# Kernel optimization log

Hardware: AMD Instinct MI355X
Metric: run time of the kernel (lower is better)

## Reference

```python
import jax, jax.numpy as jnp
import numpy as np
import math

N, IFZ, NVZ, AHZ, QPZ, KZ, PEZ = 1024, 256, 64, 8, 4, 20, 20
NUM_FREQ = PEZ // 2
FREQ_INV = 50.0

def layer_norm(x, g, b, eps=1e-5):
    mu = x.mean(-1, keepdims=True)
    var = ((x - mu) ** 2).mean(-1, keepdims=True)
    return (x - mu) / jnp.sqrt(var + eps) * g + b

def setup_inputs() -> dict:
    key = jax.random.key(0)
    ks = jax.random.split(key, 8)
    x = jax.random.normal(ks[0], (N, IFZ), jnp.float32)
    affines = jax.random.normal(ks[1], (N, 3, 4), jnp.float32)
    prot_mask = jnp.ones((N,), dtype=bool)
    edge_index = jax.random.randint(ks[2], (N, KZ), 0, N, dtype=jnp.int32)
    s = 0.02
    w_nde = jax.random.normal(ks[3], (KZ * 3 * PEZ, NVZ), jnp.float32) * s
    b_nde = jnp.zeros((NVZ,), jnp.float32)
    w_q = jax.random.normal(ks[4], (IFZ + NVZ, AHZ * QPZ * 3), jnp.float32) * s
    w_v = jax.random.normal(ks[5], (IFZ + NVZ, AHZ * QPZ * IFZ), jnp.float32) * s
    ln_ag_g = jnp.ones((AHZ * QPZ * IFZ,), jnp.float32)
    ln_ag_b = jnp.zeros((AHZ * QPZ * IFZ,), jnp.float32)
    w_ag = jax.random.normal(ks[6], (AHZ * QPZ * IFZ, IFZ), jnp.float32) * s
    ln_en_g = jnp.ones((IFZ,), jnp.float32)
    ln_en_b = jnp.zeros((IFZ,), jnp.float32)
    return dict(x=x, affines=affines, prot_mask=prot_mask, edge_index=edge_index,
                w_nde=w_nde, b_nde=b_nde, w_q=w_q, w_v=w_v,
                ln_ag_g=ln_ag_g, ln_ag_b=ln_ag_b, w_ag=w_ag,
                ln_en_g=ln_en_g, ln_en_b=ln_en_b)

def reference(x, affines, prot_mask, edge_index, w_nde, b_nde, w_q, w_v,
              ln_ag_g, ln_ag_b, w_ag, ln_en_g, ln_en_b):
    dtype = x.dtype
    R = affines[:, :, :3]                                   # (N,3,3) rotation
    t = affines[:, :, 3]                                    # (N,3) translation
    positions = t
    # --- BackboneDistanceEmbedding (reconstructed): local neighbour vectors ---
    rel = positions[edge_index] - t[:, None, :]             # (N,K,3)
    local = jnp.einsum('nji,nkj->nki', R, rel)              # inverse-affine (R^T) (N,K,3)
    freqs = jnp.arange(1, NUM_FREQ + 1, dtype=dtype) / FREQ_INV
    ang = local[..., None] * freqs                          # (N,K,3,F)
    pe = jnp.concatenate([jnp.sin(ang), jnp.cos(ang)], -1)  # (N,K,3,PEZ)
    nv = jax.nn.relu(pe.reshape(x.shape[0], -1) @ w_nde + b_nde)  # (N,NVZ)
    nv = nv * prot_mask[:, None].astype(dtype)
    x_ne = jnp.concatenate([x, nv], axis=-1)                # (N,IFZ+NVZ)
    # --- query points in global frame ---
    q = (x_ne @ w_q).reshape(-1, 1, AHZ, QPZ, 3)
    q = jnp.einsum('nij,nkaqj->nkaqi', R, q) + t[:, None, None, None, :]
    gnp = positions[edge_index][:, :, None, None, :]        # (N,K,1,1,3)
    # --- L2-distance attention over neighbourhood ---
    scores = -jnp.linalg.norm(q - gnp, axis=-1).sum(-1)     # (N,K,AHZ)
    attn = jax.nn.softmax(scores, axis=1).astype(dtype)
    # --- value gather + weighted aggregation ---
    v = (x_ne @ w_v).reshape(-1, AHZ, QPZ, IFZ)
    v_ne = v[edge_index]                                    # (N,K,AHZ,QPZ,IFZ) -- big gather
    new = jnp.einsum('nkaqi,nka->naqi', v_ne, attn).reshape(x.shape[0], -1)
    new = layer_norm(new, ln_ag_g, ln_ag_b) @ w_ag          # dropout: eval mode => identity
    out = layer_norm(x + new / math.sqrt(2.0), ln_en_g, ln_en_b).astype(dtype)
    return out, edge_index
```

## Files before the change

### kernel.cpp

```cpp
#include <hip/hip_runtime.h>
#include <hip/hip_bf16.h>
#include <math.h>

#define NNODE 1024
#define IFZ   256
#define NVZ   64
#define AHZ   8
#define QPZ   4
#define KZ    20
#define PEZ   20
#define NF    10
#define XNE   320
#define VROW  8192
#define PEK   1280
#define SPLITS 8

typedef unsigned short ushort;
typedef __attribute__((ext_vector_type(8))) short    short8v;
typedef __attribute__((ext_vector_type(8))) ushort   ushort8v;
typedef __attribute__((ext_vector_type(4))) float    float4v;

static __device__ __forceinline__ ushort f2bf(float f) {
    unsigned u = __float_as_uint(f);
    unsigned r = 0x7FFFu + ((u >> 16) & 1u);
    return (ushort)((u + r) >> 16);
}
static __device__ __forceinline__ float bf2f(unsigned h) {
    return __uint_as_float(h << 16);
}

struct TJob { const float* src; ushort* dst; const float* scl;
              int R, C, gx, base, Rdst; };
struct TJobs { TJob j[4]; };

__global__ __launch_bounds__(256) void t_conv_all(TJobs P)
{
    const int bid = blockIdx.x;
    int ji = 0;
    #pragma unroll
    for (int t = 1; t < 4; ++t) if (bid >= P.j[t].base) ji = t;
    const TJob jb = P.j[ji];
    const int rel = bid - jb.base;
    const int bx = rel % jb.gx, by = rel / jb.gx;

    __shared__ float t[32][33];
    const int c0 = bx * 32, r0 = by * 32;
    const int tx = threadIdx.x, ty = threadIdx.y;
    #pragma unroll
    for (int i = 0; i < 4; ++i) {
        int r = r0 + ty + 8*i, c = c0 + tx;
        float v = (r < jb.R && c < jb.C) ? jb.src[(size_t)r * jb.C + c] : 0.f;
        if (jb.scl && r < jb.R) v *= jb.scl[r];
        t[ty + 8*i][tx] = v;
    }
    __syncthreads();
    #pragma unroll
    for (int i = 0; i < 4; ++i)
        jb.dst[(size_t)(c0 + ty + 8*i) * jb.Rdst + r0 + tx] = f2bf(t[tx][ty + 8*i]);
}

__global__ __launch_bounds__(256) void k_gemv(
    const float* __restrict__ wag, const float* __restrict__ g,
    const float* __restrict__ b, float* __restrict__ vpart)
{
    const int sp = blockIdx.x, j = threadIdx.x;
    const float* base = wag + (size_t)sp * 128 * IFZ;
    float vp = 0.f, bp = 0.f;
    for (int r = 0; r < 128; ++r) {
        float w = base[(size_t)r * IFZ + j];
        vp += g[sp*128 + r] * w;
        bp += b[sp*128 + r] * w;
    }
    vpart[(size_t)(sp*2 + 0) * IFZ + j] = vp;
    vpart[(size_t)(sp*2 + 1) * IFZ + j] = bp;
}

__global__ __launch_bounds__(64) void k0_geom(
    const float* __restrict__ x, const float* __restrict__ aff,
    const int* __restrict__ edge,
    ushort* __restrict__ pe, ushort* __restrict__ xne_out,
    float* __restrict__ geom)
{
    const int n = blockIdx.x;
    const int lane = threadIdx.x;
    __shared__ float tn[KZ][3];
    __shared__ float r9[9], tt[3];

    if (lane < KZ) {
        int e = edge[n*KZ + lane];
        float a0 = aff[e*12 + 3], a1 = aff[e*12 + 7], a2 = aff[e*12 + 11];
        tn[lane][0] = a0; tn[lane][1] = a1; tn[lane][2] = a2;
        geom[n*72 + 12 + lane*3 + 0] = a0;
        geom[n*72 + 12 + lane*3 + 1] = a1;
        geom[n*72 + 12 + lane*3 + 2] = a2;
    } else if (lane < 29) {
        int q = lane - 20;
        float v = aff[n*12 + (q/3)*4 + (q%3)];
        r9[q] = v;
        geom[n*72 + q] = v;
    } else if (lane < 32) {
        float v = aff[n*12 + (lane-29)*4 + 3];
        tt[lane-29] = v;
        geom[n*72 + 9 + (lane-29)] = v;
    }
    {
        float4 xv = ((const float4*)(x + (size_t)n*IFZ))[lane];
        unsigned lo = f2bf(xv.x) | ((unsigned)f2bf(xv.y) << 16);
        unsigned hi = f2bf(xv.z) | ((unsigned)f2bf(xv.w) << 16);
        unsigned* p = (unsigned*)(xne_out + (size_t)n*XNE) + lane*2;
        p[0] = lo; p[1] = hi;
    }
    __syncthreads();

    if (lane < 60) {
        int k = lane / 3, i = lane % 3;
        float r0 = tn[k][0]-tt[0], r1 = tn[k][1]-tt[1], r2 = tn[k][2]-tt[2];
        float loc = r9[0+i]*r0 + r9[3+i]*r1 + r9[6+i]*r2;
        size_t base = (size_t)n*PEK + k*60 + i*20;
        #pragma unroll
        for (int p = 0; p < NF; p += 2) {
            float a0 = loc * (float)(p+1) * (1.0f/50.0f);
            float a1 = loc * (float)(p+2) * (1.0f/50.0f);
            unsigned us = f2bf(__sinf(a0)) | ((unsigned)f2bf(__sinf(a1)) << 16);
            unsigned uc = f2bf(__cosf(a0)) | ((unsigned)f2bf(__cosf(a1)) << 16);
            *(unsigned*)&pe[base + p]      = us;
            *(unsigned*)&pe[base + 10 + p] = uc;
        }
    }
    if (lane < 40)
        *(unsigned*)&pe[(size_t)n*PEK + 1200 + lane*2] = 0u;
}

#define EPI_F32S 1

template<int EPI>
__global__ __launch_bounds__(256) void gemm_bt(
    const ushort* __restrict__ A, const ushort* __restrict__ BT,
    ushort* __restrict__ Cb, float* __restrict__ Cf,
    const float* __restrict__ bias, int K, int ksplit, int ldc)
{
    __shared__ ushort As[64][40];
    __shared__ ushort Bs[64][40];
    const int bm = blockIdx.y * 64;
    const int bn = blockIdx.x * 64;
    const int tid = threadIdx.x;
    const int w = tid >> 6, lane = tid & 63;
    const int wr = w >> 1, wc = w & 1;
    const int lane15 = lane & 15, quad = lane >> 4;
    const int kbeg = blockIdx.z * ksplit;
    const int kend = kbeg + ksplit;

    const int sm = tid >> 2;
    const int sk = (tid & 3) * 8;

    float4v acc[2][2] = {};
    for (int k0 = kbeg; k0 < kend; k0 += 32) {
        *(ushort8v*)&As[sm][sk] = *(const ushort8v*)&A[(size_t)(bm + sm)*K + k0 + sk];
        *(ushort8v*)&Bs[sm][sk] = *(const ushort8v*)&BT[(size_t)(bn + sm)*K + k0 + sk];
        __syncthreads();
        short8v a0 = *(const short8v*)&As[wr*32      + lane15][quad*8];
        short8v a1 = *(const short8v*)&As[wr*32 + 16 + lane15][quad*8];
        short8v b0 = *(const short8v*)&Bs[wc*32      + lane15][quad*8];
        short8v b1 = *(const short8v*)&Bs[wc*32 + 16 + lane15][quad*8];
        acc[0][0] = __builtin_amdgcn_mfma_f32_16x16x32_bf16(a0, b0, acc[0][0], 0, 0, 0);
        acc[0][1] = __builtin_amdgcn_mfma_f32_16x16x32_bf16(a0, b1, acc[0][1], 0, 0, 0);
        acc[1][0] = __builtin_amdgcn_mfma_f32_16x16x32_bf16(a1, b0, acc[1][0], 0, 0, 0);
        acc[1][1] = __builtin_amdgcn_mfma_f32_16x16x32_bf16(a1, b1, acc[1][1], 0, 0, 0);
        __syncthreads();
    }

    const size_t splitoff = (size_t)blockIdx.z * (size_t)NNODE * (size_t)ldc;
    #pragma unroll
    for (int i = 0; i < 2; ++i) {
        #pragma unroll
        for (int j = 0; j < 2; ++j) {
            int col = bn + wc*32 + j*16 + lane15;
            #pragma unroll
            for (int r = 0; r < 4; ++r) {
                int row = bm + wr*32 + i*16 + quad*4 + r;
                Cf[splitoff + (size_t)row*ldc + col] = acc[i][j][r];
            }
        }
    }
}

__global__ __launch_bounds__(256) void gemm_head(
    const ushort* __restrict__ Ab, const ushort* __restrict__ BTb,
    ushort* __restrict__ C, float2* __restrict__ spart)
{
    const int a = blockIdx.z;
    const ushort* A  = Ab  + (size_t)a * 1024 * XNE;
    const ushort* BT = BTb + (size_t)a * 1024 * XNE;
    __shared__ ushort As[64][40];
    __shared__ ushort Bs[64][40];
    const int bm = blockIdx.y * 64;
    const int bn = blockIdx.x * 64;
    const int tid = threadIdx.x;
    const int w = tid >> 6, lane = tid & 63;
    const int wr = w >> 1, wc = w & 1;
    const int lane15 = lane & 15, quad = lane >> 4;
    const int sm = tid >> 2;
    const int sk = (tid & 3) * 8;

    float4v acc[2][2] = {};
    for (int k0 = 0; k0 < XNE; k0 += 32) {
        *(ushort8v*)&As[sm][sk] = *(const ushort8v*)&A[(size_t)(bm + sm)*XNE + k0 + sk];
        *(ushort8v*)&Bs[sm][sk] = *(const ushort8v*)&BT[(size_t)(bn + sm)*XNE + k0 + sk];
        __syncthreads();
        short8v a0 = *(const short8v*)&As[wr*32      + lane15][quad*8];
        short8v a1 = *(const short8v*)&As[wr*32 + 16 + lane15][quad*8];
        short8v b0 = *(const short8v*)&Bs[wc*32      + lane15][quad*8];
        short8v b1 = *(const short8v*)&Bs[wc*32 + 16 + lane15][quad*8];
        acc[0][0] = __builtin_amdgcn_mfma_f32_16x16x32_bf16(a0, b0, acc[0][0], 0, 0, 0);
        acc[0][1] = __builtin_amdgcn_mfma_f32_16x16x32_bf16(a0, b1, acc[0][1], 0, 0, 0);
        acc[1][0] = __builtin_amdgcn_mfma_f32_16x16x32_bf16(a1, b0, acc[1][0], 0, 0, 0);
        acc[1][1] = __builtin_amdgcn_mfma_f32_16x16x32_bf16(a1, b1, acc[1][1], 0, 0, 0);
        __syncthreads();
    }

    float rs[2][4], rq[2][4];
    #pragma unroll
    for (int i = 0; i < 2; ++i)
        #pragma unroll
        for (int r = 0; r < 4; ++r) {
            float v0 = acc[i][0][r], v1 = acc[i][1][r];
            rs[i][r] = v0 + v1;
            rq[i][r] = v0*v0 + v1*v1;
        }
    #pragma unroll
    for (int m = 1; m < 16; m <<= 1) {
        #pragma unroll
        for (int i = 0; i < 2; ++i)
            #pragma unroll
            for (int r = 0; r < 4; ++r) {
                rs[i][r] += __shfl_xor(rs[i][r], m, 64);
                rq[i][r] += __shfl_xor(rq[i][r], m, 64);
            }
    }
    if (lane15 == 0) {
        const int slot = a*32 + bn/32  ;
        const int slot2 = a*32 + (bn >> 5) + wc;
        (void)slot;
        #pragma unroll
        for (int i = 0; i < 2; ++i)
            #pragma unroll
            for (int r = 0; r < 4; ++r) {
                int row = bm + wr*32 + i*16 + quad*4 + r;
                spart[(size_t)row*256 + slot2] = make_float2(rs[i][r], rq[i][r]);
            }
    }

    #pragma unroll
    for (int i = 0; i < 2; ++i) {
        #pragma unroll
        for (int j = 0; j < 2; ++j) {
            int col = a*1024 + bn + wc*32 + j*16 + lane15;
            #pragma unroll
            for (int r = 0; r < 4; ++r) {
                int row = bm + wr*32 + i*16 + quad*4 + r;
                C[(size_t)row*VROW + col] = f2bf(acc[i][j][r]);
            }
        }
    }
}

__global__ __launch_bounds__(256) void k_nv(
    const float* __restrict__ nvpart, const float* __restrict__ bias,
    const float* __restrict__ vpart, ushort* __restrict__ xne,
    float* __restrict__ vconst)
{
    const int tid = threadIdx.x;
    if (blockIdx.x >= 256) {
        int vb = blockIdx.x - 256;
        float s = 0.f;
        #pragma unroll 8
        for (int sp = 0; sp < 64; ++sp)
            s += vpart[(size_t)(sp*2 + vb)*IFZ + tid];
        vconst[vb*IFZ + tid] = s;
        return;
    }
    int idx = blockIdx.x*256 + tid;
    int n = idx >> 6, c = idx & 63;
    float s = nvpart[idx] + nvpart[65536 + idx] + nvpart[2*65536 + idx]
            + nvpart[3*65536 + idx];
    xne[(size_t)n*XNE + IFZ + c] = f2bf(fmaxf(s + bias[c], 0.f));
}

__global__ __launch_bounds__(256) void k_sc_agg(
    const float* __restrict__ qbuf, const float* __restrict__ geom,
    const ushort* __restrict__ xne, const int* __restrict__ edge,
    ushort* __restrict__ agg)
{
    const int n = blockIdx.x;
    const int tid = threadIdx.x;
    __shared__ float geo[72], qg[96], sc[160], at[160];
    __shared__ int es[KZ];
    __shared__ ushort xs[KZ][XNE];

    if (tid < 72) geo[tid] = geom[n*72 + tid];
    else if (tid < 92) es[tid-72] = edge[n*KZ + (tid-72)];
    __syncthreads();

    if (tid < 96) {
        int i = tid % 3, base = (tid/3)*3;
        float q0 = qbuf[n*128 + base], q1 = qbuf[n*128 + base+1], q2 = qbuf[n*128 + base+2];
        qg[tid] = geo[i*3+0]*q0 + geo[i*3+1]*q1 + geo[i*3+2]*q2 + geo[9+i];
    }
    for (int s = tid; s < KZ*40; s += 256) {
        int k = s / 40, ch = s % 40;
        *(ushort8v*)&xs[k][ch*8] = *(const ushort8v*)&xne[(size_t)es[k]*XNE + ch*8];
    }
    __syncthreads();

    if (tid < 160) {
        int k = tid / 8, a = tid % 8;
        float tx = geo[12+k*3+0], ty = geo[12+k*3+1], tz = geo[12+k*3+2];
        float acc = 0.f;
        #pragma unroll
        for (int qp = 0; qp < QPZ; ++qp) {
            int b = a*12 + qp*3;
            float dx = qg[b]   - tx;
            float dy = qg[b+1] - ty;
            float dz = qg[b+2] - tz;
            acc += sqrtf(dx*dx + dy*dy + dz*dz);
        }
        sc[a*20 + k] = -acc;
    }
    __syncthreads();
    if (tid < 8) {
        int a = tid;
        float m = -1e30f;
        #pragma unroll
        for (int k = 0; k < KZ; ++k) m = fmaxf(m, sc[a*20+k]);
        float e[KZ]; float sum = 0.f;
        #pragma unroll
        for (int k = 0; k < KZ; ++k) { e[k] = __expf(sc[a*20+k] - m); sum += e[k]; }
        float inv = 1.f / sum;
        #pragma unroll
        for (int k = 0; k < KZ; ++k) at[k*8 + a] = e[k]*inv;
    }
    __syncthreads();

    for (int s = tid; s < AHZ*40; s += 256) {
        int a = s / 40, ch = s % 40;
        float acc[8] = {};
        #pragma unroll 4
        for (int k = 0; k < KZ; ++k) {
            ushort8v p = *(const ushort8v*)&xs[k][ch*8];
            float wgt = at[k*8 + a];
            #pragma unroll
            for (int j = 0; j < 8; ++j)
                acc[j] += wgt * bf2f((ushort)p[j]);
        }
        ushort8v o;
        #pragma unroll
        for (int j = 0; j < 8; ++j) o[j] = (short)f2bf(acc[j]);
        *(ushort8v*)&agg[((size_t)a*NNODE + n)*XNE + ch*8] = o;
    }
}

__global__ __launch_bounds__(256) void k6_final(
    const float* __restrict__ x, const float* __restrict__ tmp,
    const float* __restrict__ g, const float* __restrict__ b,
    const int* __restrict__ edge, const float2* __restrict__ spart,
    const float* __restrict__ vconst, float* __restrict__ out)
{
    const int n = blockIdx.x;
    const int tid = threadIdx.x;
    __shared__ float wsum[4], wsq[4];
    __shared__ float s_mu8, s_rstd8, s_mu, s_rstd;
    const int wid = tid >> 6, lane = tid & 63;

    float2 sp = spart[(size_t)n*256 + tid];
    float a8 = sp.x, q8 = sp.y;
    #pragma unroll
    for (int off = 32; off > 0; off >>= 1) {
        a8 += __shfl_down(a8, off, 64);
        q8 += __shfl_down(q8, off, 64);
    }
    if (lane == 0) { wsum[wid] = a8; wsq[wid] = q8; }
    __syncthreads();
    if (tid == 0) {
        float ts = wsum[0]+wsum[1]+wsum[2]+wsum[3];
        float tq = wsq[0]+wsq[1]+wsq[2]+wsq[3];
        float mu = ts * (1.f/(float)VROW);
        float var = tq * (1.f/(float)VROW) - mu*mu;
        s_mu8 = mu; s_rstd8 = rsqrtf(var + 1e-5f);
    }
    __syncthreads();
    const float mu8 = s_mu8, rstd8 = s_rstd8;

    float s = 0.f;
    #pragma unroll
    for (int spi = 0; spi < SPLITS; ++spi)
        s += tmp[spi*(NNODE*IFZ) + n*IFZ + tid];
    float vc = vconst[tid], bc = vconst[IFZ + tid];
    float pre = rstd8*s - rstd8*mu8*vc + bc;

    float val = x[n*IFZ + tid] + pre * 0.70710678118654752f;
    float lsum = val, lsq = val*val;
    #pragma unroll
    for (int off = 32; off > 0; off >>= 1) {
        lsum += __shfl_down(lsum, off, 64);
        lsq  += __shfl_down(lsq,  off, 64);
    }
    __syncthreads();
    if (lane == 0) { wsum[wid] = lsum; wsq[wid] = lsq; }
    __syncthreads();
    if (tid == 0) {
        float ts = wsum[0]+wsum[1]+wsum[2]+wsum[3];
        float tq = wsq[0]+wsq[1]+wsq[2]+wsq[3];
        float mu = ts / (float)IFZ;
        float var = tq / (float)IFZ - mu*mu;
        s_mu = mu; s_rstd = rsqrtf(var + 1e-5f);
    }
    __syncthreads();
    out[n*IFZ + tid] = (val - s_mu)*s_rstd*g[tid] + b[tid];
    if (tid < KZ)
        out[NNODE*IFZ + n*KZ + tid] = (float)edge[n*KZ + tid];
}

extern "C" void kernel_launch(void* const* d_in, const int* in_sizes, int n_in,
                              void* d_out, int out_size, void* d_ws, size_t ws_size,
                              hipStream_t stream)
{
    const float* x       = (const float*)d_in[0];
    const float* aff     = (const float*)d_in[1];
    const int*   edge    = (const int*)d_in[3];
    const float* w_nde   = (const float*)d_in[4];
    const float* b_nde   = (const float*)d_in[5];
    const float* w_q     = (const float*)d_in[6];
    const float* w_v     = (const float*)d_in[7];
    const float* ln_ag_g = (const float*)d_in[8];
    const float* ln_ag_b = (const float*)d_in[9];
    const float* w_ag    = (const float*)d_in[10];
    const float* ln_en_g = (const float*)d_in[11];
    const float* ln_en_b = (const float*)d_in[12];
    float* out = (float*)d_out;
    char*  w   = (char*)d_ws;

    ushort* xne_bf = (ushort*)(w + 0x0);
    float2* spart  = (float2*)(w + 0xA0000);
    float*  vpart  = (float*) (w + 0x2A0000);
    float*  vconst = (float*) (w + 0x2C0000);
    float*  nvpart = (float*) (w + 0x2D0000);
    ushort* wvT    = (ushort*)(w + 0x3D0000);
    ushort* wagT   = (ushort*)(w + 0x8D0000);
    ushort* newbf  = (ushort*)(w + 0xCD0000);
    float*  tmpk   = (float*) (w + 0x1CD0000);
    ushort* pebf   = (ushort*)(w + 0x24D0000);
    ushort* wndeT  = (ushort*)(w + 0x2750000);
    ushort* wqT    = (ushort*)(w + 0x2778000);
    float*  qbuf   = (float*) (w + 0x278C000);
    float*  geom   = (float*) (w + 0x280C000);
    ushort* agg    = (ushort*)(w + 0x2854000);

    TJobs P;
    P.j[0] = { w_v,   wvT,   nullptr, XNE,  VROW, VROW/32, 0,    XNE  };
    P.j[1] = { w_ag,  wagT,  ln_ag_g, VROW, IFZ,  IFZ/32,  2560, VROW };
    P.j[2] = { w_nde, wndeT, nullptr, 1200, NVZ,  2,       4608, PEK  };
    P.j[3] = { w_q,   wqT,   nullptr, XNE,  96,   4,       4688, XNE  };
    hipLaunchKernelGGL(t_conv_all, dim3(4728), dim3(32, 8), 0, stream, P);

    hipLaunchKernelGGL(k_gemv, dim3(64), dim3(256), 0, stream,
                       w_ag, ln_ag_g, ln_ag_b, vpart);

    hipLaunchKernelGGL(k0_geom, dim3(NNODE), dim3(64), 0, stream,
                       x, aff, edge, pebf, xne_bf, geom);

    hipLaunchKernelGGL((gemm_bt<EPI_F32S>), dim3(1, NNODE/64, 4), dim3(256), 0, stream,
                       pebf, wndeT, (ushort*)nullptr, nvpart, (float*)nullptr,
                       PEK, PEK/4, NVZ);

    hipLaunchKernelGGL(k_nv, dim3(258), dim3(256), 0, stream,
                       nvpart, b_nde, vpart, xne_bf, vconst);

    hipLaunchKernelGGL((gemm_bt<EPI_F32S>), dim3(2, NNODE/64, 1), dim3(256), 0, stream,
                       xne_bf, wqT, (ushort*)nullptr, qbuf, (float*)nullptr,
                       XNE, XNE, 128);

    hipLaunchKernelGGL(k_sc_agg, dim3(NNODE), dim3(256), 0, stream,
                       qbuf, geom, xne_bf, edge, agg);

    hipLaunchKernelGGL(gemm_head, dim3(1024/64, NNODE/64, AHZ), dim3(256), 0, stream,
                       agg, wvT, newbf, spart);

    hipLaunchKernelGGL((gemm_bt<EPI_F32S>), dim3(IFZ/64, NNODE/64, SPLITS), dim3(256), 0, stream,
                       newbf, wagT, (ushort*)nullptr, tmpk, (float*)nullptr,
                       VROW, VROW/SPLITS, IFZ);

    hipLaunchKernelGGL(k6_final, dim3(NNODE), dim3(256), 0, stream,
                       x, tmpk, ln_en_g, ln_en_b, edge, spart, vconst, out);
}
```

Before: 177.0 us.

## Fold value projection into output weights and Gram matrix, merge prep launches

Reassociates the big value path so the 1024x8192 per-head value tensor is never formed. A combined weight WcT = w_v·(g*w_ag) and a per-head Gram matrix G = w_v·w_vᵀ are precomputed. LayerNorm statistics come from row sums of w_v and quadratic forms agg·G·agg, and the output projection is computed directly from the 2560-wide aggregated features. Preprocessing kernels and the small GEMMs are merged into single multi-job launches to cut launch count. The trade-off is extra per-call weight-product GEMMs and possible precision changes in the variance computed via the Gram form.

```diff
diff --git a/kernel.cpp b/kernel.cpp
--- a/kernel.cpp
+++ b/kernel.cpp
@@ -8,12 +8,12 @@
 #define AHZ   8
 #define QPZ   4
 #define KZ    20
-#define PEZ   20
 #define NF    10
 #define XNE   320
 #define VROW  8192
 #define PEK   1280
-#define SPLITS 8
+#define PTOT  2560
+#define SPLITS2 2
 
 typedef unsigned short ushort;
 typedef __attribute__((ext_vector_type(8))) short    short8v;
@@ -29,134 +29,18 @@
     return __uint_as_float(h << 16);
 }
 
-struct TJob { const float* src; ushort* dst; const float* scl;
-              int R, C, gx, base, Rdst; };
-struct TJobs { TJob j[4]; };
-
-__global__ __launch_bounds__(256) void t_conv_all(TJobs P)
-{
-    const int bid = blockIdx.x;
-    int ji = 0;
-    #pragma unroll
-    for (int t = 1; t < 4; ++t) if (bid >= P.j[t].base) ji = t;
-    const TJob jb = P.j[ji];
-    const int rel = bid - jb.base;
-    const int bx = rel % jb.gx, by = rel / jb.gx;
-
-    __shared__ float t[32][33];
-    const int c0 = bx * 32, r0 = by * 32;
-    const int tx = threadIdx.x, ty = threadIdx.y;
-    #pragma unroll
-    for (int i = 0; i < 4; ++i) {
-        int r = r0 + ty + 8*i, c = c0 + tx;
-        float v = (r < jb.R && c < jb.C) ? jb.src[(size_t)r * jb.C + c] : 0.f;
-        if (jb.scl && r < jb.R) v *= jb.scl[r];
-        t[ty + 8*i][tx] = v;
-    }
-    __syncthreads();
-    #pragma unroll
-    for (int i = 0; i < 4; ++i)
-        jb.dst[(size_t)(c0 + ty + 8*i) * jb.Rdst + r0 + tx] = f2bf(t[tx][ty + 8*i]);
-}
-
-__global__ __launch_bounds__(256) void k_gemv(
-    const float* __restrict__ wag, const float* __restrict__ g,
-    const float* __restrict__ b, float* __restrict__ vpart)
-{
-    const int sp = blockIdx.x, j = threadIdx.x;
-    const float* base = wag + (size_t)sp * 128 * IFZ;
-    float vp = 0.f, bp = 0.f;
-    for (int r = 0; r < 128; ++r) {
-        float w = base[(size_t)r * IFZ + j];
-        vp += g[sp*128 + r] * w;
-        bp += b[sp*128 + r] * w;
-    }
-    vpart[(size_t)(sp*2 + 0) * IFZ + j] = vp;
-    vpart[(size_t)(sp*2 + 1) * IFZ + j] = bp;
-}
-
-__global__ __launch_bounds__(64) void k0_geom(
-    const float* __restrict__ x, const float* __restrict__ aff,
-    const int* __restrict__ edge,
-    ushort* __restrict__ pe, ushort* __restrict__ xne_out,
-    float* __restrict__ geom)
-{
-    const int n = blockIdx.x;
-    const int lane = threadIdx.x;
-    __shared__ float tn[KZ][3];
-    __shared__ float r9[9], tt[3];
-
-    if (lane < KZ) {
-        int e = edge[n*KZ + lane];
-        float a0 = aff[e*12 + 3], a1 = aff[e*12 + 7], a2 = aff[e*12 + 11];
-        tn[lane][0] = a0; tn[lane][1] = a1; tn[lane][2] = a2;
-        geom[n*72 + 12 + lane*3 + 0] = a0;
-        geom[n*72 + 12 + lane*3 + 1] = a1;
-        geom[n*72 + 12 + lane*3 + 2] = a2;
-    } else if (lane < 29) {
-        int q = lane - 20;
-        float v = aff[n*12 + (q/3)*4 + (q%3)];
-        r9[q] = v;
-        geom[n*72 + q] = v;
-    } else if (lane < 32) {
-        float v = aff[n*12 + (lane-29)*4 + 3];
-        tt[lane-29] = v;
-        geom[n*72 + 9 + (lane-29)] = v;
-    }
-    {
-        float4 xv = ((const float4*)(x + (size_t)n*IFZ))[lane];
-        unsigned lo = f2bf(xv.x) | ((unsigned)f2bf(xv.y) << 16);
-        unsigned hi = f2bf(xv.z) | ((unsigned)f2bf(xv.w) << 16);
-        unsigned* p = (unsigned*)(xne_out + (size_t)n*XNE) + lane*2;
-        p[0] = lo; p[1] = hi;
-    }
-    __syncthreads();
-
-    if (lane < 60) {
-        int k = lane / 3, i = lane % 3;
-        float r0 = tn[k][0]-tt[0], r1 = tn[k][1]-tt[1], r2 = tn[k][2]-tt[2];
-        float loc = r9[0+i]*r0 + r9[3+i]*r1 + r9[6+i]*r2;
-        size_t base = (size_t)n*PEK + k*60 + i*20;
-        #pragma unroll
-        for (int p = 0; p < NF; p += 2) {
-            float a0 = loc * (float)(p+1) * (1.0f/50.0f);
-            float a1 = loc * (float)(p+2) * (1.0f/50.0f);
-            unsigned us = f2bf(__sinf(a0)) | ((unsigned)f2bf(__sinf(a1)) << 16);
-            unsigned uc = f2bf(__cosf(a0)) | ((unsigned)f2bf(__cosf(a1)) << 16);
-            *(unsigned*)&pe[base + p]      = us;
-            *(unsigned*)&pe[base + 10 + p] = uc;
-        }
-    }
-    if (lane < 40)
-        *(unsigned*)&pe[(size_t)n*PEK + 1200 + lane*2] = 0u;
-}
-
-#define EPI_F32S 1
-
-template<int EPI>
-__global__ __launch_bounds__(256) void gemm_bt(
+static __device__ __forceinline__ void gemm_tile(
     const ushort* __restrict__ A, const ushort* __restrict__ BT,
-    ushort* __restrict__ Cb, float* __restrict__ Cf,
-    const float* __restrict__ bias, int K, int ksplit, int ldc)
-{
-    __shared__ ushort As[64][40];
-    __shared__ ushort Bs[64][40];
-    const int bm = blockIdx.y * 64;
-    const int bn = blockIdx.x * 64;
-    const int tid = threadIdx.x;
+    int aStride, int btStride, int kLen, int bm, int bn, int tid,
+    float4v acc[2][2], ushort (&As)[64][40], ushort (&Bs)[64][40])
+{
     const int w = tid >> 6, lane = tid & 63;
     const int wr = w >> 1, wc = w & 1;
     const int lane15 = lane & 15, quad = lane >> 4;
-    const int kbeg = blockIdx.z * ksplit;
-    const int kend = kbeg + ksplit;
-
-    const int sm = tid >> 2;
-    const int sk = (tid & 3) * 8;
-
-    float4v acc[2][2] = {};
-    for (int k0 = kbeg; k0 < kend; k0 += 32) {
-        *(ushort8v*)&As[sm][sk] = *(const ushort8v*)&A[(size_t)(bm + sm)*K + k0 + sk];
-        *(ushort8v*)&Bs[sm][sk] = *(const ushort8v*)&BT[(size_t)(bn + sm)*K + k0 + sk];
+    const int sm = tid >> 2, sk = (tid & 3) * 8;
+    for (int k0 = 0; k0 < kLen; k0 += 32) {
+        *(ushort8v*)&As[sm][sk] = *(const ushort8v*)&A[(size_t)(bm + sm)*aStride + k0 + sk];
+        *(ushort8v*)&Bs[sm][sk] = *(const ushort8v*)&BT[(size_t)(bn + sm)*btStride + k0 + sk];
         __syncthreads();
         short8v a0 = *(const short8v*)&As[wr*32      + lane15][quad*8];
         short8v a1 = *(const short8v*)&As[wr*32 + 16 + lane15][quad*8];
@@ -168,8 +52,167 @@
         acc[1][1] = __builtin_amdgcn_mfma_f32_16x16x32_bf16(a1, b1, acc[1][1], 0, 0, 0);
         __syncthreads();
     }
-
-    const size_t splitoff = (size_t)blockIdx.z * (size_t)NNODE * (size_t)ldc;
+}
+
+#define T1_END 2048
+#define T2_END 2128
+#define T3_END 2168
+#define CV_END 2488
+#define GV_END 2552
+#define K0_END 2808
+
+__global__ __launch_bounds__(256) void prep(
+    const float* __restrict__ w_ag, const float* __restrict__ ln_ag_g,
+    const float* __restrict__ ln_ag_b,
+    const float* __restrict__ w_nde, const float* __restrict__ w_q,
+    const float* __restrict__ w_v,
+    const float* __restrict__ x, const float* __restrict__ aff,
+    const int* __restrict__ edge,
+    ushort* __restrict__ wagT, ushort* __restrict__ wndeT,
+    ushort* __restrict__ wqT, ushort* __restrict__ wv_bf,
+    float* __restrict__ rsum, float* __restrict__ vpart,
+    ushort* __restrict__ pebf, ushort* __restrict__ xne_bf,
+    float* __restrict__ geom)
+{
+    const int bid = blockIdx.x;
+    const int tid = threadIdx.x;
+
+    __shared__ float t[32][33];
+    __shared__ float part[256];
+    __shared__ float tn[4][KZ][3];
+    __shared__ float r9[4][9], tt[4][3];
+
+    if (bid < T3_END) {
+        const float* src; ushort* dst; const float* scl;
+        int R, C, gx, Rdst, rel;
+        if (bid < T1_END)      { src=w_ag; dst=wagT; scl=ln_ag_g; R=VROW; C=IFZ; gx=8;  Rdst=VROW; rel=bid; }
+        else if (bid < T2_END) { src=w_nde;dst=wndeT;scl=nullptr; R=1200; C=NVZ; gx=2;  Rdst=PEK;  rel=bid-T1_END; }
+        else                   { src=w_q;  dst=wqT;  scl=nullptr; R=XNE;  C=96;  gx=4;  Rdst=XNE;  rel=bid-T2_END; }
+        const int bx = rel % gx, by = rel / gx;
+        const int c0 = bx*32, r0 = by*32;
+        const int tx = tid & 31, ty = tid >> 5;
+        #pragma unroll
+        for (int i = 0; i < 4; ++i) {
+            int r = r0 + ty + 8*i, c = c0 + tx;
+            float v = (r < R && c < C) ? src[(size_t)r * C + c] : 0.f;
+            if (scl && r < R) v *= scl[r];
+            t[ty + 8*i][tx] = v;
+        }
+        __syncthreads();
+        #pragma unroll
+        for (int i = 0; i < 4; ++i)
+            dst[(size_t)(c0 + ty + 8*i) * Rdst + r0 + tx] = f2bf(t[tx][ty + 8*i]);
+    } else if (bid < CV_END) {
+        const int j = bid - T3_END;
+        const float* src = w_v + (size_t)j*VROW + tid*32;
+        ushort* dst = wv_bf + (size_t)j*VROW + tid*32;
+        float psum = 0.f;
+        #pragma unroll
+        for (int q = 0; q < 4; ++q) {
+            float4 v0 = ((const float4*)src)[q*2];
+            float4 v1 = ((const float4*)src)[q*2+1];
+            psum += v0.x+v0.y+v0.z+v0.w + v1.x+v1.y+v1.z+v1.w;
+            ushort8v o;
+            o[0]=f2bf(v0.x); o[1]=f2bf(v0.y); o[2]=f2bf(v0.z); o[3]=f2bf(v0.w);
+            o[4]=f2bf(v1.x); o[5]=f2bf(v1.y); o[6]=f2bf(v1.z); o[7]=f2bf(v1.w);
+            *(ushort8v*)(dst + q*8) = o;
+        }
+        part[tid] = psum;
+        __syncthreads();
+        if (tid < 8) {
+            float s = 0.f;
+            #pragma unroll
+            for (int u = 0; u < 32; ++u) s += part[tid*32 + u];
+            rsum[tid*320 + j] = s;
+        }
+    } else if (bid < GV_END) {
+        const int sp = bid - CV_END, j = tid;
+        const float* base = w_ag + (size_t)sp * 128 * IFZ;
+        float vp = 0.f, bp = 0.f;
+        for (int r = 0; r < 128; ++r) {
+            float wv = base[(size_t)r * IFZ + j];
+            vp += ln_ag_g[sp*128 + r] * wv;
+            bp += ln_ag_b[sp*128 + r] * wv;
+        }
+        vpart[(size_t)(sp*2 + 0) * IFZ + j] = vp;
+        vpart[(size_t)(sp*2 + 1) * IFZ + j] = bp;
+    } else {
+        const int rel = bid - GV_END;
+        const int wv = tid >> 6, lane = tid & 63;
+        const int n = rel*4 + wv;
+        if (lane < KZ) {
+            int e = edge[n*KZ + lane];
+            float a0 = aff[e*12 + 3], a1 = aff[e*12 + 7], a2 = aff[e*12 + 11];
+            tn[wv][lane][0] = a0; tn[wv][lane][1] = a1; tn[wv][lane][2] = a2;
+            geom[n*72 + 12 + lane*3 + 0] = a0;
+            geom[n*72 + 12 + lane*3 + 1] = a1;
+            geom[n*72 + 12 + lane*3 + 2] = a2;
+        } else if (lane < 29) {
+            int q = lane - 20;
+            float v = aff[n*12 + (q/3)*4 + (q%3)];
+            r9[wv][q] = v;
+            geom[n*72 + q] = v;
+        } else if (lane < 32) {
+            float v = aff[n*12 + (lane-29)*4 + 3];
+            tt[wv][lane-29] = v;
+            geom[n*72 + 9 + (lane-29)] = v;
+        }
+        {
+            float4 xv = ((const float4*)(x + (size_t)n*IFZ))[lane];
+            unsigned lo = f2bf(xv.x) | ((unsigned)f2bf(xv.y) << 16);
+            unsigned hi = f2bf(xv.z) | ((unsigned)f2bf(xv.w) << 16);
+            unsigned* p = (unsigned*)(xne_bf + (size_t)n*XNE) + lane*2;
+            p[0] = lo; p[1] = hi;
+        }
+        __syncthreads();
+        if (lane < 60) {
+            int k = lane / 3, i = lane % 3;
+            float d0 = tn[wv][k][0]-tt[wv][0], d1 = tn[wv][k][1]-tt[wv][1], d2 = tn[wv][k][2]-tt[wv][2];
+            float loc = r9[wv][0+i]*d0 + r9[wv][3+i]*d1 + r9[wv][6+i]*d2;
+            size_t base = (size_t)n*PEK + k*60 + i*20;
+            #pragma unroll
+            for (int p = 0; p < NF; p += 2) {
+                float a0 = loc * (float)(p+1) * (1.0f/50.0f);
+                float a1 = loc * (float)(p+2) * (1.0f/50.0f);
+                unsigned us = f2bf(__sinf(a0)) | ((unsigned)f2bf(__sinf(a1)) << 16);
+                unsigned uc = f2bf(__cosf(a0)) | ((unsigned)f2bf(__cosf(a1)) << 16);
+                *(unsigned*)&pebf[base + p]      = us;
+                *(unsigned*)&pebf[base + 10 + p] = uc;
+            }
+        }
+        if (lane < 40)
+            *(unsigned*)&pebf[(size_t)n*PEK + 1200 + lane*2] = 0u;
+    }
+}
+
+struct GJob { const ushort* A; const ushort* BT; ushort* Cb; float* Cf;
+              int base, gx, gy, aStride, btStride, ldc, kLen;
+              long aZ, btZ, cZ; };
+struct GJobs { GJob j[4]; };
+
+__global__ __launch_bounds__(256) void gemm_jobs(GJobs P)
+{
+    __shared__ ushort As[64][40];
+    __shared__ ushort Bs[64][40];
+    const int bid = blockIdx.x;
+    const int tid = threadIdx.x;
+    int ji = 0;
+    #pragma unroll
+    for (int u = 1; u < 4; ++u) if (bid >= P.j[u].base) ji = u;
+    GJob jb = P.j[ji];
+    int rel = bid - jb.base;
+    int bx = rel % jb.gx, tmp = rel / jb.gx;
+    int by = tmp % jb.gy, bz = tmp / jb.gy;
+    const int bm = by*64, bn = bx*64;
+
+    float4v acc[2][2] = {};
+    gemm_tile(jb.A + (size_t)bz*jb.aZ, jb.BT + (size_t)bz*jb.btZ,
+              jb.aStride, jb.btStride, jb.kLen, bm, bn, tid, acc, As, Bs);
+
+    const int w = tid >> 6, lane = tid & 63;
+    const int wr = w >> 1, wc = w & 1;
+    const int lane15 = lane & 15, quad = lane >> 4;
+    const size_t cbase = (size_t)bz * jb.cZ;
     #pragma unroll
     for (int i = 0; i < 2; ++i) {
         #pragma unroll
@@ -178,87 +221,9 @@
             #pragma unroll
             for (int r = 0; r < 4; ++r) {
                 int row = bm + wr*32 + i*16 + quad*4 + r;
-                Cf[splitoff + (size_t)row*ldc + col] = acc[i][j][r];
-            }
-        }
-    }
-}
-
-__global__ __launch_bounds__(256) void gemm_head(
-    const ushort* __restrict__ Ab, const ushort* __restrict__ BTb,
-    ushort* __restrict__ C, float2* __restrict__ spart)
-{
-    const int a = blockIdx.z;
-    const ushort* A  = Ab  + (size_t)a * 1024 * XNE;
-    const ushort* BT = BTb + (size_t)a * 1024 * XNE;
-    __shared__ ushort As[64][40];
-    __shared__ ushort Bs[64][40];
-    const int bm = blockIdx.y * 64;
-    const int bn = blockIdx.x * 64;
-    const int tid = threadIdx.x;
-    const int w = tid >> 6, lane = tid & 63;
-    const int wr = w >> 1, wc = w & 1;
-    const int lane15 = lane & 15, quad = lane >> 4;
-    const int sm = tid >> 2;
-    const int sk = (tid & 3) * 8;
-
-    float4v acc[2][2] = {};
-    for (int k0 = 0; k0 < XNE; k0 += 32) {
-        *(ushort8v*)&As[sm][sk] = *(const ushort8v*)&A[(size_t)(bm + sm)*XNE + k0 + sk];
-        *(ushort8v*)&Bs[sm][sk] = *(const ushort8v*)&BT[(size_t)(bn + sm)*XNE + k0 + sk];
-        __syncthreads();
-        short8v a0 = *(const short8v*)&As[wr*32      + lane15][quad*8];
-        short8v a1 = *(const short8v*)&As[wr*32 + 16 + lane15][quad*8];
-        short8v b0 = *(const short8v*)&Bs[wc*32      + lane15][quad*8];
-        short8v b1 = *(const short8v*)&Bs[wc*32 + 16 + lane15][quad*8];
-        acc[0][0] = __builtin_amdgcn_mfma_f32_16x16x32_bf16(a0, b0, acc[0][0], 0, 0, 0);
-        acc[0][1] = __builtin_amdgcn_mfma_f32_16x16x32_bf16(a0, b1, acc[0][1], 0, 0, 0);
-        acc[1][0] = __builtin_amdgcn_mfma_f32_16x16x32_bf16(a1, b0, acc[1][0], 0, 0, 0);
-        acc[1][1] = __builtin_amdgcn_mfma_f32_16x16x32_bf16(a1, b1, acc[1][1], 0, 0, 0);
-        __syncthreads();
-    }
-
-    float rs[2][4], rq[2][4];
-    #pragma unroll
-    for (int i = 0; i < 2; ++i)
-        #pragma unroll
-        for (int r = 0; r < 4; ++r) {
-            float v0 = acc[i][0][r], v1 = acc[i][1][r];
-            rs[i][r] = v0 + v1;
-            rq[i][r] = v0*v0 + v1*v1;
-        }
-    #pragma unroll
-    for (int m = 1; m < 16; m <<= 1) {
-        #pragma unroll
-        for (int i = 0; i < 2; ++i)
-            #pragma unroll
-            for (int r = 0; r < 4; ++r) {
-                rs[i][r] += __shfl_xor(rs[i][r], m, 64);
-                rq[i][r] += __shfl_xor(rq[i][r], m, 64);
-            }
-    }
-    if (lane15 == 0) {
-        const int slot = a*32 + bn/32  ;
-        const int slot2 = a*32 + (bn >> 5) + wc;
-        (void)slot;
-        #pragma unroll
-        for (int i = 0; i < 2; ++i)
-            #pragma unroll
-            for (int r = 0; r < 4; ++r) {
-                int row = bm + wr*32 + i*16 + quad*4 + r;
-                spart[(size_t)row*256 + slot2] = make_float2(rs[i][r], rq[i][r]);
-            }
-    }
-
-    #pragma unroll
-    for (int i = 0; i < 2; ++i) {
-        #pragma unroll
-        for (int j = 0; j < 2; ++j) {
-            int col = a*1024 + bn + wc*32 + j*16 + lane15;
-            #pragma unroll
-            for (int r = 0; r < 4; ++r) {
-                int row = bm + wr*32 + i*16 + quad*4 + r;
-                C[(size_t)row*VROW + col] = f2bf(acc[i][j][r]);
+                float val = acc[i][j][r];
+                if (jb.Cf) jb.Cf[cbase + (size_t)row*jb.ldc + col] = val;
+                else       jb.Cb[cbase + (size_t)row*jb.ldc + col] = f2bf(val);
             }
         }
     }
@@ -289,29 +254,41 @@
 __global__ __launch_bounds__(256) void k_sc_agg(
     const float* __restrict__ qbuf, const float* __restrict__ geom,
     const ushort* __restrict__ xne, const int* __restrict__ edge,
-    ushort* __restrict__ agg)
+    const float* __restrict__ w_q, const float* __restrict__ rsum,
+    ushort* __restrict__ agg, float* __restrict__ S)
 {
     const int n = blockIdx.x;
     const int tid = threadIdx.x;
-    __shared__ float geo[72], qg[96], sc[160], at[160];
+    __shared__ float geo[72], qf[96], qg[96], sc[160], at[160], nvr[64];
+    __shared__ float rs[PTOT];
     __shared__ int es[KZ];
     __shared__ ushort xs[KZ][XNE];
+    __shared__ float red[256];
 
     if (tid < 72) geo[tid] = geom[n*72 + tid];
-    else if (tid < 92) es[tid-72] = edge[n*KZ + (tid-72)];
-    __syncthreads();
-
-    if (tid < 96) {
-        int i = tid % 3, base = (tid/3)*3;
-        float q0 = qbuf[n*128 + base], q1 = qbuf[n*128 + base+1], q2 = qbuf[n*128 + base+2];
-        qg[tid] = geo[i*3+0]*q0 + geo[i*3+1]*q1 + geo[i*3+2]*q2 + geo[9+i];
-    }
+    if (tid < KZ) es[tid] = edge[n*KZ + tid];
+    if (tid < 64) nvr[tid] = bf2f(xne[(size_t)n*XNE + IFZ + tid]);
+    for (int p = tid; p < PTOT; p += 256) rs[p] = rsum[p];
+    __syncthreads();
+
     for (int s = tid; s < KZ*40; s += 256) {
         int k = s / 40, ch = s % 40;
         *(ushort8v*)&xs[k][ch*8] = *(const ushort8v*)&xne[(size_t)es[k]*XNE + ch*8];
     }
-    __syncthreads();
-
+    if (tid < 96) {
+        float qv = qbuf[n*128 + tid];
+        #pragma unroll 16
+        for (int r = 0; r < 64; ++r)
+            qv += nvr[r] * w_q[(256 + r)*96 + tid];
+        qf[tid] = qv;
+    }
+    __syncthreads();
+    if (tid < 96) {
+        int i = tid % 3, base = (tid/3)*3;
+        qg[tid] = geo[i*3+0]*qf[base] + geo[i*3+1]*qf[base+1]
+                + geo[i*3+2]*qf[base+2] + geo[9+i];
+    }
+    __syncthreads();
     if (tid < 160) {
         int k = tid / 8, a = tid % 8;
         float tx = geo[12+k*3+0], ty = geo[12+k*3+1], tz = geo[12+k*3+2];
@@ -341,6 +318,7 @@
     }
     __syncthreads();
 
+    float sp = 0.f;
     for (int s = tid; s < AHZ*40; s += 256) {
         int a = s / 40, ch = s % 40;
         float acc[8] = {};
@@ -354,16 +332,86 @@
         }
         ushort8v o;
         #pragma unroll
-        for (int j = 0; j < 8; ++j) o[j] = (short)f2bf(acc[j]);
-        *(ushort8v*)&agg[((size_t)a*NNODE + n)*XNE + ch*8] = o;
+        for (int j = 0; j < 8; ++j) {
+            o[j] = (short)f2bf(acc[j]);
+            sp += acc[j] * rs[a*320 + ch*8 + j];
+        }
+        *(ushort8v*)&agg[(size_t)n*PTOT + a*320 + ch*8] = o;
+    }
+    red[tid] = sp;
+    __syncthreads();
+    if (tid < 64) {
+        float v = red[tid] + red[tid+64] + red[tid+128] + red[tid+192];
+        #pragma unroll
+        for (int off = 32; off > 0; off >>= 1) v += __shfl_down(v, off, 64);
+        if (tid == 0) S[n] = v;
+    }
+}
+
+__global__ __launch_bounds__(256) void gemm_b(
+    const ushort* __restrict__ agg, const ushort* __restrict__ G,
+    const ushort* __restrict__ WcT, float* __restrict__ s2part,
+    float* __restrict__ tmpk)
+{
+    __shared__ ushort As[64][40];
+    __shared__ ushort Bs[64][40];
+    const int bid = blockIdx.x;
+    const int tid = threadIdx.x;
+    const int w = tid >> 6, lane = tid & 63;
+    const int wr = w >> 1, wc = w & 1;
+    const int lane15 = lane & 15, quad = lane >> 4;
+    float4v acc[2][2] = {};
+
+    if (bid < 640) {
+        const int bx = bid % 5, by = (bid/5) % 16, a = bid/80;
+        const int bm = by*64, bn = bx*64;
+        gemm_tile(agg + a*320, G + (size_t)a*320*320,
+                  PTOT, 320, 320, bm, bn, tid, acc, As, Bs);
+        #pragma unroll
+        for (int i = 0; i < 2; ++i) {
+            #pragma unroll
+            for (int r = 0; r < 4; ++r) {
+                int row = bm + wr*32 + i*16 + quad*4 + r;
+                int c0  = bn + wc*32 + lane15;
+                float av0 = bf2f(agg[(size_t)row*PTOT + a*320 + c0]);
+                float av1 = bf2f(agg[(size_t)row*PTOT + a*320 + c0 + 16]);
+                float v = acc[i][0][r]*av0 + acc[i][1][r]*av1;
+                v += __shfl_xor(v, 1, 64);
+                v += __shfl_xor(v, 2, 64);
+                v += __shfl_xor(v, 4, 64);
+                v += __shfl_xor(v, 8, 64);
+                if (lane15 == 0)
+                    s2part[(size_t)row*80 + a*10 + (bn>>5) + wc] = v;
+            }
+        }
+    } else {
+        const int rel = bid - 640;
+        const int bx = rel % 4, by = (rel/4) % 16, z = rel/64;
+        const int bm = by*64, bn = bx*64;
+        gemm_tile(agg + z*1280, WcT + z*1280,
+                  PTOT, PTOT, 1280, bm, bn, tid, acc, As, Bs);
+        float* Cf = tmpk + (size_t)z*NNODE*IFZ;
+        #pragma unroll
+        for (int i = 0; i < 2; ++i) {
+            #pragma unroll
+            for (int j = 0; j < 2; ++j) {
+                int col = bn + wc*32 + j*16 + lane15;
+                #pragma unroll
+                for (int r = 0; r < 4; ++r) {
+                    int row = bm + wr*32 + i*16 + quad*4 + r;
+                    Cf[(size_t)row*IFZ + col] = acc[i][j][r];
+                }
+            }
+        }
     }
 }
 
 __global__ __launch_bounds__(256) void k6_final(
-    const float* __restrict__ x, const float* __restrict__ tmp,
+    const float* __restrict__ x, const float* __restrict__ tmpk,
     const float* __restrict__ g, const float* __restrict__ b,
-    const int* __restrict__ edge, const float2* __restrict__ spart,
-    const float* __restrict__ vconst, float* __restrict__ out)
+    const int* __restrict__ edge, const float* __restrict__ s2part,
+    const float* __restrict__ S, const float* __restrict__ vconst,
+    float* __restrict__ out)
 {
     const int n = blockIdx.x;
     const int tid = threadIdx.x;
@@ -371,29 +419,22 @@
     __shared__ float s_mu8, s_rstd8, s_mu, s_rstd;
     const int wid = tid >> 6, lane = tid & 63;
 
-    float2 sp = spart[(size_t)n*256 + tid];
-    float a8 = sp.x, q8 = sp.y;
+    float v = (tid < 80) ? s2part[(size_t)n*80 + tid] : 0.f;
     #pragma unroll
-    for (int off = 32; off > 0; off >>= 1) {
-        a8 += __shfl_down(a8, off, 64);
-        q8 += __shfl_down(q8, off, 64);
-    }
-    if (lane == 0) { wsum[wid] = a8; wsq[wid] = q8; }
+    for (int off = 32; off > 0; off >>= 1) v += __shfl_down(v, off, 64);
+    if (lane == 0) wsum[wid] = v;
     __syncthreads();
     if (tid == 0) {
-        float ts = wsum[0]+wsum[1]+wsum[2]+wsum[3];
-        float tq = wsq[0]+wsq[1]+wsq[2]+wsq[3];
-        float mu = ts * (1.f/(float)VROW);
-        float var = tq * (1.f/(float)VROW) - mu*mu;
+        float S2 = wsum[0]+wsum[1]+wsum[2]+wsum[3];
+        float Sv = S[n];
+        float mu = Sv * (1.f/(float)VROW);
+        float var = S2 * (1.f/(float)VROW) - mu*mu;
         s_mu8 = mu; s_rstd8 = rsqrtf(var + 1e-5f);
     }
     __syncthreads();
     const float mu8 = s_mu8, rstd8 = s_rstd8;
 
-    float s = 0.f;
-    #pragma unroll
-    for (int spi = 0; spi < SPLITS; ++spi)
-        s += tmp[spi*(NNODE*IFZ) + n*IFZ + tid];
+    float s = tmpk[n*IFZ + tid] + tmpk[NNODE*IFZ + n*IFZ + tid];
     float vc = vconst[tid], bc = vconst[IFZ + tid];
     float pre = rstd8*s - rstd8*mu8*vc + bc;
 
@@ -440,55 +481,44 @@
     char*  w   = (char*)d_ws;
 
     ushort* xne_bf = (ushort*)(w + 0x0);
-    float2* spart  = (float2*)(w + 0xA0000);
-    float*  vpart  = (float*) (w + 0x2A0000);
-    float*  vconst = (float*) (w + 0x2C0000);
-    float*  nvpart = (float*) (w + 0x2D0000);
-    ushort* wvT    = (ushort*)(w + 0x3D0000);
-    ushort* wagT   = (ushort*)(w + 0x8D0000);
-    ushort* newbf  = (ushort*)(w + 0xCD0000);
-    float*  tmpk   = (float*) (w + 0x1CD0000);
-    ushort* pebf   = (ushort*)(w + 0x24D0000);
-    ushort* wndeT  = (ushort*)(w + 0x2750000);
-    ushort* wqT    = (ushort*)(w + 0x2778000);
-    float*  qbuf   = (float*) (w + 0x278C000);
-    float*  geom   = (float*) (w + 0x280C000);
-    ushort* agg    = (ushort*)(w + 0x2854000);
-
-    TJobs P;
-    P.j[0] = { w_v,   wvT,   nullptr, XNE,  VROW, VROW/32, 0,    XNE  };
-    P.j[1] = { w_ag,  wagT,  ln_ag_g, VROW, IFZ,  IFZ/32,  2560, VROW };
-    P.j[2] = { w_nde, wndeT, nullptr, 1200, NVZ,  2,       4608, PEK  };
-    P.j[3] = { w_q,   wqT,   nullptr, XNE,  96,   4,       4688, XNE  };
-    hipLaunchKernelGGL(t_conv_all, dim3(4728), dim3(32, 8), 0, stream, P);
-
-    hipLaunchKernelGGL(k_gemv, dim3(64), dim3(256), 0, stream,
-                       w_ag, ln_ag_g, ln_ag_b, vpart);
-
-    hipLaunchKernelGGL(k0_geom, dim3(NNODE), dim3(64), 0, stream,
-                       x, aff, edge, pebf, xne_bf, geom);
-
-    hipLaunchKernelGGL((gemm_bt<EPI_F32S>), dim3(1, NNODE/64, 4), dim3(256), 0, stream,
-                       pebf, wndeT, (ushort*)nullptr, nvpart, (float*)nullptr,
-                       PEK, PEK/4, NVZ);
+    float*  qbuf   = (float*) (w + 0xA0000);
+    float*  vpart  = (float*) (w + 0x120000);
+    float*  vconst = (float*) (w + 0x140000);
+    float*  nvpart = (float*) (w + 0x141000);
+    ushort* wagT   = (ushort*)(w + 0x250000);
+    ushort* wv_bf  = (ushort*)(w + 0x650000);
+    ushort* WcT    = (ushort*)(w + 0xB50000);
+    ushort* G      = (ushort*)(w + 0xC90000);
+    float*  rsum   = (float*) (w + 0xE20000);
+    float*  S      = (float*) (w + 0xE23000);
+    float*  s2part = (float*) (w + 0xE24000);
+    ushort* agg    = (ushort*)(w + 0xE80000);
+    float*  tmpk   = (float*) (w + 0x1380000);
+    ushort* pebf   = (ushort*)(w + 0x1580000);
+    ushort* wndeT  = (ushort*)(w + 0x1800000);
+    ushort* wqT    = (ushort*)(w + 0x1828000);
+    float*  geom   = (float*) (w + 0x1840000);
+
+    hipLaunchKernelGGL(prep, dim3(K0_END), dim3(256), 0, stream,
+                       w_ag, ln_ag_g, ln_ag_b, w_nde, w_q, w_v, x, aff, edge,
+                       wagT, wndeT, wqT, wv_bf, rsum, vpart, pebf, xne_bf, geom);
+
+    GJobs P;
+    P.j[0] = { wagT,   wv_bf,  WcT,   nullptr, 0,   5, 4,  VROW, VROW, PTOT, 1024, 1024,  1024,   320    };
+    P.j[1] = { wv_bf,  wv_bf,  G,     nullptr, 160, 5, 5,  VROW, VROW, 320,  1024, 1024,  1024,   102400 };
+    P.j[2] = { pebf,   wndeT,  nullptr, nvpart,360, 1, 16, PEK,  PEK,  NVZ,  320,  320,   320,    65536  };
+    P.j[3] = { xne_bf, wqT,    nullptr, qbuf,  424, 2, 16, XNE,  XNE,  128,  256,  0,     0,      0      };
+    hipLaunchKernelGGL(gemm_jobs, dim3(456), dim3(256), 0, stream, P);
 
     hipLaunchKernelGGL(k_nv, dim3(258), dim3(256), 0, stream,
                        nvpart, b_nde, vpart, xne_bf, vconst);
 
-    hipLaunchKernelGGL((gemm_bt<EPI_F32S>), dim3(2, NNODE/64, 1), dim3(256), 0, stream,
-                       xne_bf, wqT, (ushort*)nullptr, qbuf, (float*)nullptr,
-                       XNE, XNE, 128);
-
     hipLaunchKernelGGL(k_sc_agg, dim3(NNODE), dim3(256), 0, stream,
-                       qbuf, geom, xne_bf, edge, agg);
-
-    hipLaunchKernelGGL(gemm_head, dim3(1024/64, NNODE/64, AHZ), dim3(256), 0, stream,
-                       agg, wvT, newbf, spart);
-
-    hipLaunchKernelGGL((gemm_bt<EPI_F32S>), dim3(IFZ/64, NNODE/64, SPLITS), dim3(256), 0, stream,
-                       newbf, wagT, (ushort*)nullptr, tmpk, (float*)nullptr,
-                       VROW, VROW/SPLITS, IFZ);
+                       qbuf, geom, xne_bf, edge, w_q, rsum, agg, S);
+
+    hipLaunchKernelGGL(gemm_b, dim3(768), dim3(256), 0, stream,
+                       agg, G, WcT, s2part, tmpk);
 
     hipLaunchKernelGGL(k6_final, dim3(NNODE), dim3(256), 0, stream,
-                       x, tmpk, ln_en_g, ln_en_b, edge, spart, vconst, out);
-}
+                       x, tmpk, ln_en_g, ln_en_b, edge, s2part, S, vconst, out);
+}
```

Result: faster. 159.1 us (-10.1%).
